# Performance work log

Hardware: AMD Instinct MI355X
Metric: run time of the kernel (lower is better)

The kernel has to match this reference:

```python
import jax, jax.numpy as jnp
import numpy as np

B, N, D, H, C = 8, 1024, 1024, 8, 1
S = 32            # sqrt(D // C): per-patch spatial map side
HD = D // H       # head dim = 128
SCALE = HD ** -0.5
BN_EPS = 1e-3     # Keras BatchNormalization default epsilon


def setup_inputs() -> dict:
    key = jax.random.key(0)
    ks = jax.random.split(key, 7)
    std = 0.02  # matches tf.random_normal_initializer(0.0, 0.02)
    return {
        "x": jax.random.normal(ks[0], (B, N, D), jnp.float32),
        "qw": jax.random.normal(ks[1], (3, 3, C, C), jnp.float32) * std,
        "kw": jax.random.normal(ks[2], (3, 3, C, C), jnp.float32) * std,
        "vw": jax.random.normal(ks[3], (3, 3, C, C), jnp.float32) * std,
        "reatten_w": jax.random.normal(ks[4], (N, N), jnp.float32) / np.float32(np.sqrt(N)),
        "reatten_b": jnp.zeros((N,), jnp.float32),
        "bn_gamma": jnp.ones((N,), jnp.float32),
        "bn_beta": jnp.zeros((N,), jnp.float32),
        "proj_w": jax.random.normal(ks[5], (D, D), jnp.float32) / np.float32(np.sqrt(D)),
        "proj_b": jnp.zeros((D,), jnp.float32),
    }


def _conv_qkv(x, w):
    # unflatten: [B, N, D] -> [B*N, S, S, C]; map_fn over batch with a shared
    # conv == one conv with B*N as batch dim. 3x3 SAME, no bias, exact GELU.
    xm = x.reshape(B * N, S, S, C)
    y = jax.lax.conv_general_dilated(
        xm, w, window_strides=(1, 1), padding='SAME',
        dimension_numbers=('NHWC', 'HWIO', 'NHWC'))
    y = jax.nn.gelu(y, approximate=False)
    # reshape to heads: [B, N, H, HD] -> [B, H, N, HD]
    return y.reshape(B, N, H, HD).transpose(0, 2, 1, 3)


def reference(x, qw, kw, vw, reatten_w, reatten_b, bn_gamma, bn_beta, proj_w, proj_b):
    q = _conv_qkv(x, qw)
    k = _conv_qkv(x, kw)
    v = _conv_qkv(x, vw)

    attn = jax.nn.softmax(jnp.einsum('bhid,bhjd->bhij', q, k) * SCALE, axis=-1)
    # re-attention: 1x1 conv over last (key) axis + BN (inference: mean=0, var=1)
    attn = jnp.einsum('bhic,cj->bhij', attn, reatten_w) + reatten_b
    attn = attn * (bn_gamma / jnp.sqrt(jnp.float32(1.0) + BN_EPS)) + bn_beta
    # reatten_scale = 1.0 (transform_scale=False)

    out = jnp.einsum('bhij,bhjd->bhid', attn, v)
    out = out.transpose(0, 2, 1, 3).reshape(B, N, D)
    out = out @ proj_w + proj_b
    return (out, attn)
```

## Files before the change

kernel.cpp:

```cpp
#include <hip/hip_runtime.h>
#include <hip/hip_bf16.h>

typedef __attribute__((ext_vector_type(8))) short short8;
typedef __attribute__((ext_vector_type(4))) float f32x4;

__device__ __forceinline__ void gload_lds16(const void* g, void* l) {
    __builtin_amdgcn_global_load_lds(
        (const __attribute__((address_space(1))) void*)g,
        (__attribute__((address_space(3))) void*)l, 16, 0, 0);
}

#define SBAR() do { __builtin_amdgcn_sched_barrier(0); __builtin_amdgcn_s_barrier(); __builtin_amdgcn_sched_barrier(0); } while (0)

__device__ __forceinline__ float gelu_exact(float x) {
    return 0.5f * x * (1.0f + erff(x * 0.70710678118654752f));
}
__device__ __forceinline__ float us2f(unsigned int u) {
    return __uint_as_float(u << 16);
}
__device__ __forceinline__ unsigned short f2b_raw(float f) {
    __hip_bfloat16 h = __float2bfloat16(f);
    return *reinterpret_cast<unsigned short*>(&h);
}
__device__ __forceinline__ float tofloat(float f) { return f; }
__device__ __forceinline__ float tofloat(__hip_bfloat16 h) { return __bfloat162float(h); }

__global__ __launch_bounds__(256) void conv_qkv(
    const float* __restrict__ x,
    const float* __restrict__ qw, const float* __restrict__ kw, const float* __restrict__ vw,
    __hip_bfloat16* __restrict__ qb, __hip_bfloat16* __restrict__ kb, __hip_bfloat16* __restrict__ vb)
{
    __shared__ float img[1024];
    const int bid = blockIdx.x;
    const int b = bid >> 10, n = bid & 1023;
    const float* xr = x + (long)bid * 1024;
    for (int i = threadIdx.x; i < 1024; i += 256) img[i] = xr[i];
    __syncthreads();

    float wq[9], wk[9], wv[9];
    #pragma unroll
    for (int i = 0; i < 9; ++i) { wq[i] = qw[i]; wk[i] = kw[i]; wv[i] = vw[i]; }

    for (int q = 0; q < 4; ++q) {
        const int p = q * 256 + threadIdx.x;
        const int r = p >> 5, c = p & 31;
        float sq = 0.f, sk = 0.f, sv = 0.f;
        #pragma unroll
        for (int dy = 0; dy < 3; ++dy) {
            const int rr = r + dy - 1;
            if (rr < 0 || rr > 31) continue;
            #pragma unroll
            for (int dx = 0; dx < 3; ++dx) {
                const int cc = c + dx - 1;
                if (cc < 0 || cc > 31) continue;
                const float px = img[rr * 32 + cc];
                sq += px * wq[dy * 3 + dx];
                sk += px * wk[dy * 3 + dx];
                sv += px * wv[dy * 3 + dx];
            }
        }
        sq = gelu_exact(sq); sk = gelu_exact(sk); sv = gelu_exact(sv);
        const int h = p >> 7, d = p & 127;
        const long off = ((long)(b * 8 + h) * 1024 + n) * 128 + d;
        qb[off] = __float2bfloat16(sq);
        kb[off] = __float2bfloat16(sk);
        vb[off] = __float2bfloat16(sv);
    }
}

template <typename Tin>
__global__ __launch_bounds__(256) void transpose_cast(
    const Tin* __restrict__ in, __hip_bfloat16* __restrict__ out,
    int R, int Cc, long inz, long outz)
{
    __shared__ float tile[32][33];
    const long z = blockIdx.z;
    const int c0 = blockIdx.x * 32, r0 = blockIdx.y * 32;
    const int tx = threadIdx.x & 31, ty = threadIdx.x >> 5;
    const Tin* ip = in + z * inz;
    #pragma unroll
    for (int i = 0; i < 32; i += 8)
        tile[ty + i][tx] = tofloat(ip[(long)(r0 + ty + i) * Cc + (c0 + tx)]);
    __syncthreads();
    __hip_bfloat16* op = out + z * outz;
    #pragma unroll
    for (int i = 0; i < 32; i += 8)
        op[(long)(c0 + ty + i) * R + (r0 + tx)] = __float2bfloat16(tile[tx][ty + i]);
}

__global__ __launch_bounds__(256) void softmax_inplace(__hip_bfloat16* __restrict__ S)
{
    __shared__ float red[8];
    const long row = blockIdx.x;
    uint2* p = reinterpret_cast<uint2*>(S + row * 1024);
    const int tid = threadIdx.x;
    uint2 u = p[tid];
    float v0 = us2f(u.x & 0xffffu), v1 = us2f(u.x >> 16);
    float v2 = us2f(u.y & 0xffffu), v3 = us2f(u.y >> 16);

    float m = fmaxf(fmaxf(v0, v1), fmaxf(v2, v3));
    for (int o = 32; o; o >>= 1) m = fmaxf(m, __shfl_xor(m, o));
    const int wave = tid >> 6, lane = tid & 63;
    if (lane == 0) red[wave] = m;
    __syncthreads();
    m = fmaxf(fmaxf(red[0], red[1]), fmaxf(red[2], red[3]));

    float e0 = expf(v0 - m), e1 = expf(v1 - m), e2 = expf(v2 - m), e3 = expf(v3 - m);
    float s = e0 + e1 + e2 + e3;
    for (int o = 32; o; o >>= 1) s += __shfl_xor(s, o);
    if (lane == 0) red[4 + wave] = s;
    __syncthreads();
    s = red[4] + red[5] + red[6] + red[7];
    const float inv = 1.0f / s;

    u.x = (unsigned int)f2b_raw(e0 * inv) | ((unsigned int)f2b_raw(e1 * inv) << 16);
    u.y = (unsigned int)f2b_raw(e2 * inv) | ((unsigned int)f2b_raw(e3 * inv) << 16);
    p[tid] = u;
}

__global__ __launch_bounds__(512, 2) void gemm_reatten_256(
    const __hip_bfloat16* __restrict__ Sall, const __hip_bfloat16* __restrict__ Wt,
    float* __restrict__ Cout,
    const float* __restrict__ bg, const float* __restrict__ rb, const float* __restrict__ bb)
{
    __shared__ __align__(16) char smem[131072];
    char* ldsA = smem;
    char* ldsB = smem + 65536;

    const int tid = threadIdx.x;
    const int z = blockIdx.z, tileM = blockIdx.x, tileN = blockIdx.y;
    const char* Ab = (const char*)(Sall + (long)z * 1048576 + (long)tileM * 256 * 1024);
    const char* Bb = (const char*)(Wt + (long)tileN * 256 * 1024);

    int grow[2], goff[2], pphys[2];
    #pragma unroll
    for (int i = 0; i < 2; ++i) {
        const int p = i * 8192 + tid * 16;
        const int l = p ^ (((p >> 7) & 3) << 4);
        pphys[i] = p; grow[i] = l >> 6; goff[i] = l & 63;
    }
    auto STAGE = [&](const char* gb, char* lb, int kt) {
        #pragma unroll
        for (int i = 0; i < 2; ++i)
            gload_lds16(gb + (long)grow[i] * 2048 + kt * 64 + goff[i], lb + pphys[i]);
    };

    const int lane = tid & 63, wid = tid >> 6;
    const int wrM = wid >> 2, wcn = wid & 3;
    const int fr = lane & 15, kl = lane >> 4;
    const int frbase = fr * 64 + kl * 16;

    auto LD8 = [&](const char* buf, int L) -> short8 {
        const int ph = L ^ (((L >> 7) & 3) << 4);
        return *(const short8*)(buf + ph);
    };

    f32x4 acc[8][4];
    #pragma unroll
    for (int m = 0; m < 8; ++m)
        #pragma unroll
        for (int n = 0; n < 4; ++n) acc[m][n] = (f32x4){0.f, 0.f, 0.f, 0.f};

    STAGE(Ab, ldsA, 0);          STAGE(Bb, ldsB, 0);
    STAGE(Ab, ldsA + 16384, 1);  STAGE(Bb, ldsB + 16384, 1);
    asm volatile("s_waitcnt vmcnt(4)" ::: "memory");
    SBAR();

    #pragma unroll 1
    for (int t = 0; t < 32; ++t) {
        char* bufA = ldsA + (t & 3) * 16384;
        char* bufB = ldsB + (t & 3) * 16384;
        const int t2 = t + 2;
        char* nA = ldsA + (t2 & 3) * 16384;
        char* nB = ldsB + (t2 & 3) * 16384;

        short8 bf[4], af[4];
        #pragma unroll
        for (int n = 0; n < 4; ++n) bf[n] = LD8(bufB, ((wcn * 64 + n * 16) * 64) + frbase);
        #pragma unroll
        for (int j = 0; j < 4; ++j) af[j] = LD8(bufA, ((wrM * 128 + j * 16) * 64) + frbase);
        if (t2 < 32) STAGE(Ab, nA, t2);
        SBAR();
        asm volatile("s_waitcnt lgkmcnt(0)" ::: "memory");
        __builtin_amdgcn_sched_barrier(0);
        __builtin_amdgcn_s_setprio(1);
        #pragma unroll
        for (int j = 0; j < 4; ++j)
            #pragma unroll
            for (int n = 0; n < 4; ++n)
                acc[j][n] = __builtin_amdgcn_mfma_f32_16x16x32_bf16(af[j], bf[n], acc[j][n], 0, 0, 0);
        __builtin_amdgcn_s_setprio(0);
        SBAR();

        #pragma unroll
        for (int j = 0; j < 4; ++j) af[j] = LD8(bufA, ((wrM * 128 + 64 + j * 16) * 64) + frbase);
        if (t2 < 32) STAGE(Bb, nB, t2);
        SBAR();
        asm volatile("s_waitcnt lgkmcnt(0)" ::: "memory");
        __builtin_amdgcn_sched_barrier(0);
        __builtin_amdgcn_s_setprio(1);
        #pragma unroll
        for (int j = 0; j < 4; ++j)
            #pragma unroll
            for (int n = 0; n < 4; ++n)
                acc[4 + j][n] = __builtin_amdgcn_mfma_f32_16x16x32_bf16(af[j], bf[n], acc[4 + j][n], 0, 0, 0);
        __builtin_amdgcn_s_setprio(0);
        if (t < 30)       asm volatile("s_waitcnt vmcnt(4)" ::: "memory");
        else if (t == 30) asm volatile("s_waitcnt vmcnt(0)" ::: "memory");
        SBAR();
    }

    __syncthreads();
    float* cbuf = (float*)smem;
    const float bninv = rsqrtf(1.0f + 1e-3f);
    float alpha[4], addv[4];
    #pragma unroll
    for (int n = 0; n < 4; ++n) {
        const int col = tileN * 256 + wcn * 64 + n * 16 + fr;
        const float g = bg[col];
        alpha[n] = g * bninv;
        addv[n] = rb[col] * alpha[n] + bb[col];
    }
    const int srow = tid >> 3, cseg = (tid & 7) * 4;
    #pragma unroll
    for (int c = 0; c < 4; ++c) {
        if (wrM == (c >> 1)) {
            #pragma unroll
            for (int j = 0; j < 4; ++j) {
                const int mf = (c & 1) * 4 + j;
                const int lrow0 = j * 16 + kl * 4;
                #pragma unroll
                for (int n = 0; n < 4; ++n)
                    #pragma unroll
                    for (int r = 0; r < 4; ++r)
                        cbuf[(lrow0 + r) * 260 + wcn * 64 + n * 16 + fr] =
                            acc[mf][n][r] * alpha[n] + addv[n];
            }
        }
        __syncthreads();
        float* gptr = Cout + (long)z * 1048576 +
                      (long)(tileM * 256 + c * 64 + srow) * 1024 + tileN * 256;
        #pragma unroll
        for (int i = 0; i < 8; ++i)
            *(f32x4*)(gptr + cseg + i * 32) = *(const f32x4*)&cbuf[srow * 260 + cseg + i * 32];
        __syncthreads();
    }
}

template <int MODE>
__global__ __launch_bounds__(256) void gemm_nt(
    const void* __restrict__ Aall, const __hip_bfloat16* __restrict__ Ball,
    void* __restrict__ Call, int K,
    long sAz, long sBz, long sCz,
    const float* __restrict__ e0)
{
    constexpr bool AF32 = (MODE == 2);
    constexpr bool OF32 = (MODE == 3);

    __shared__ __align__(16) char smem[32 * 132 * 4];
    short* As = (short*)smem;
    short* Bs = (short*)(smem + 8192);
    float* cbuf = (float*)smem;

    const int tid = threadIdx.x;
    const int z = blockIdx.z;
    const int tileM = blockIdx.x, tileN = blockIdx.y;

    const short* AwB = nullptr;
    const float* AwF = nullptr;
    if constexpr (AF32) AwF = (const float*)Aall + sAz * z + (long)tileM * 128 * K;
    else                AwB = (const short*)Aall + sAz * z + (long)tileM * 128 * K;
    const short* Bw = (const short*)Ball + sBz * z + (long)tileN * 128 * K;

    const int r0s = tid >> 2, k0s = (tid & 3) * 8;
    const int r1s = r0s + 64;

    f32x4 acc[4][4];
    #pragma unroll
    for (int m = 0; m < 4; ++m)
        #pragma unroll
        for (int n = 0; n < 4; ++n) acc[m][n] = (f32x4){0.f, 0.f, 0.f, 0.f};

    const int lane = tid & 63;
    const int wave = tid >> 6;
    const int wr = (wave >> 1) * 64, wc = (wave & 1) * 64;
    const int fr = lane & 15;
    const int kb = (lane >> 4) * 8;

    const int nk = K >> 5;
    for (int kt = 0; kt < nk; ++kt) {
        if constexpr (AF32) {
            const float* Ak0 = AwF + (long)r0s * K + kt * 32 + k0s;
            const float* Ak1 = AwF + (long)r1s * K + kt * 32 + k0s;
            f32x4 a00 = *(const f32x4*)Ak0;
            f32x4 a01 = *(const f32x4*)(Ak0 + 4);
            f32x4 a10 = *(const f32x4*)Ak1;
            f32x4 a11 = *(const f32x4*)(Ak1 + 4);
            __syncthreads();
            short8 s0, s1;
            #pragma unroll
            for (int i = 0; i < 4; ++i) {
                s0[i] = (short)f2b_raw(a00[i]); s0[i + 4] = (short)f2b_raw(a01[i]);
                s1[i] = (short)f2b_raw(a10[i]); s1[i + 4] = (short)f2b_raw(a11[i]);
            }
            *(short8*)&As[tid * 8] = s0;
            *(short8*)&As[(tid + 256) * 8] = s1;
            gload_lds16(Bw + (long)r0s * K + kt * 32 + k0s, &Bs[tid * 8]);
            gload_lds16(Bw + (long)r1s * K + kt * 32 + k0s, &Bs[(tid + 256) * 8]);
            __syncthreads();
        } else {
            __syncthreads();
            gload_lds16(AwB + (long)r0s * K + kt * 32 + k0s, &As[tid * 8]);
            gload_lds16(AwB + (long)r1s * K + kt * 32 + k0s, &As[(tid + 256) * 8]);
            gload_lds16(Bw + (long)r0s * K + kt * 32 + k0s, &Bs[tid * 8]);
            gload_lds16(Bw + (long)r1s * K + kt * 32 + k0s, &Bs[(tid + 256) * 8]);
            __syncthreads();
        }

        short8 af[4], bf[4];
        #pragma unroll
        for (int m = 0; m < 4; ++m) af[m] = *(const short8*)&As[(wr + m * 16 + fr) * 32 + kb];
        #pragma unroll
        for (int n = 0; n < 4; ++n) bf[n] = *(const short8*)&Bs[(wc + n * 16 + fr) * 32 + kb];
        #pragma unroll
        for (int m = 0; m < 4; ++m)
            #pragma unroll
            for (int n = 0; n < 4; ++n)
                acc[m][n] = __builtin_amdgcn_mfma_f32_16x16x32_bf16(af[m], bf[n], acc[m][n], 0, 0, 0);
    }

    long cbase;
    if (MODE == 2) cbase = (long)(z >> 3) * 1048576 + (long)(z & 7) * 128;
    else           cbase = sCz * z;

    float alpha[4], addv[4];
    #pragma unroll
    for (int n = 0; n < 4; ++n) {
        const int col = tileN * 128 + wc + n * 16 + fr;
        float a_ = 1.f, b_ = 0.f;
        if (MODE == 0) a_ = 0.08838834764831843f;
        if (MODE == 3) b_ = e0[col];
        alpha[n] = a_; addv[n] = b_;
    }

    __syncthreads();
    #pragma unroll
    for (int q = 0; q < 4; ++q) {
        if ((wave >> 1) == (q >> 1)) {
            #pragma unroll
            for (int mm = 0; mm < 2; ++mm) {
                const int m = (q & 1) * 2 + mm;
                const int lr0 = m * 16 + (lane >> 4) * 4 - (q & 1) * 32;
                #pragma unroll
                for (int n = 0; n < 4; ++n)
                    #pragma unroll
                    for (int r = 0; r < 4; ++r)
                        cbuf[(lr0 + r) * 132 + wc + n * 16 + fr] = acc[m][n][r] * alpha[n] + addv[n];
            }
        }
        __syncthreads();
        const long growbase = (long)tileM * 128 + q * 32;
        if constexpr (OF32) {
            float* Cg = (float*)Call + cbase;
            #pragma unroll
            for (int pass = 0; pass < 4; ++pass) {
                const int idx = (tid + pass * 256) * 4;
                const int row = idx >> 7, col = idx & 127;
                f32x4 v = *(const f32x4*)&cbuf[row * 132 + col];
                *(f32x4*)&Cg[(growbase + row) * 1024 + tileN * 128 + col] = v;
            }
        } else {
            __hip_bfloat16* Cg = (__hip_bfloat16*)Call + cbase;
            #pragma unroll
            for (int pass = 0; pass < 2; ++pass) {
                const int idx = (tid + pass * 256) * 8;
                const int row = idx >> 7, col = idx & 127;
                const float* src = &cbuf[row * 132 + col];
                f32x4 v0 = *(const f32x4*)src;
                f32x4 v1 = *(const f32x4*)(src + 4);
                short8 s;
                #pragma unroll
                for (int i = 0; i < 4; ++i) {
                    s[i] = (short)f2b_raw(v0[i]);
                    s[i + 4] = (short)f2b_raw(v1[i]);
                }
                *(short8*)&Cg[(growbase + row) * 1024 + tileN * 128 + col] = s;
            }
        }
        __syncthreads();
    }
}

extern "C" void kernel_launch(void* const* d_in, const int* in_sizes, int n_in,
                              void* d_out, int out_size, void* d_ws, size_t ws_size,
                              hipStream_t stream)
{
    const float* x  = (const float*)d_in[0];
    const float* qw = (const float*)d_in[1];
    const float* kw = (const float*)d_in[2];
    const float* vw = (const float*)d_in[3];
    const float* rw = (const float*)d_in[4];
    const float* rb = (const float*)d_in[5];
    const float* bg = (const float*)d_in[6];
    const float* bb = (const float*)d_in[7];
    const float* pw = (const float*)d_in[8];
    const float* pb = (const float*)d_in[9];

    float* outF  = (float*)d_out;
    float* attnF = outF + 8388608;

    char* w = (char*)d_ws;
    __hip_bfloat16* qb    = (__hip_bfloat16*)w; w += 16777216;
    __hip_bfloat16* kb    = (__hip_bfloat16*)w; w += 16777216;
    __hip_bfloat16* vb    = (__hip_bfloat16*)w; w += 16777216;
    __hip_bfloat16* vt    = (__hip_bfloat16*)w; w += 16777216;
    __hip_bfloat16* Wt    = (__hip_bfloat16*)w; w += 2097152;
    __hip_bfloat16* pWt   = (__hip_bfloat16*)w; w += 2097152;
    __hip_bfloat16* o2    = (__hip_bfloat16*)w; w += 16777216;
    __hip_bfloat16* S     = (__hip_bfloat16*)w; w += 134217728;

    conv_qkv<<<8192, 256, 0, stream>>>(x, qw, kw, vw, qb, kb, vb);
    transpose_cast<float><<<dim3(32, 32, 1), 256, 0, stream>>>(rw, Wt, 1024, 1024, 0, 0);
    transpose_cast<float><<<dim3(32, 32, 1), 256, 0, stream>>>(pw, pWt, 1024, 1024, 0, 0);
    transpose_cast<__hip_bfloat16><<<dim3(4, 32, 64), 256, 0, stream>>>(vb, vt, 1024, 128, 131072, 131072);

    gemm_nt<0><<<dim3(8, 8, 64), 256, 0, stream>>>(
        qb, kb, S, 128, 131072, 131072, 1048576, nullptr);
    softmax_inplace<<<65536, 256, 0, stream>>>(S);
    gemm_reatten_256<<<dim3(4, 4, 64), 512, 0, stream>>>(S, Wt, attnF, bg, rb, bb);
    gemm_nt<2><<<dim3(8, 1, 64), 256, 0, stream>>>(
        attnF, vt, o2, 1024, 1048576, 131072, 0, nullptr);
    gemm_nt<3><<<dim3(64, 8, 1), 256, 0, stream>>>(
        o2, pWt, outF, 1024, 0, 0, 0, pb);
}
```

Baseline: 423.8 us.

## Emit bf16 attention copy from re-attention GEMM and trim its barriers

The re-attention GEMM epilogue now also writes a bf16 copy of the attention matrix to a new 128 MB workspace buffer. The attn@V GEMM reads that copy with asynchronous global-to-LDS loads instead of loading fp32 attention and converting it in registers, so its fp32-path code is removed. The main loop of the re-attention GEMM also drops its intermediate barriers and explicit LDS waits, keeping one barrier per k-step and holding the second A-fragment half in separate registers. In exchange the epilogue stores an extra 128 MB of bf16 data and needs more workspace and registers, and correctness now depends on the four-deep LDS ring with a single barrier per step.

```diff
diff --git a/kernel.cpp b/kernel.cpp
--- a/kernel.cpp
+++ b/kernel.cpp
@@ -9,8 +9,6 @@
         (const __attribute__((address_space(1))) void*)g,
         (__attribute__((address_space(3))) void*)l, 16, 0, 0);
 }
-
-#define SBAR() do { __builtin_amdgcn_sched_barrier(0); __builtin_amdgcn_s_barrier(); __builtin_amdgcn_sched_barrier(0); } while (0)
 
 __device__ __forceinline__ float gelu_exact(float x) {
     return 0.5f * x * (1.0f + erff(x * 0.70710678118654752f));
@@ -120,7 +118,7 @@
 
 __global__ __launch_bounds__(512, 2) void gemm_reatten_256(
     const __hip_bfloat16* __restrict__ Sall, const __hip_bfloat16* __restrict__ Wt,
-    float* __restrict__ Cout,
+    float* __restrict__ Cout, __hip_bfloat16* __restrict__ C2out,
     const float* __restrict__ bg, const float* __restrict__ rb, const float* __restrict__ bb)
 {
     __shared__ __align__(16) char smem[131072];
@@ -164,7 +162,9 @@
     STAGE(Ab, ldsA, 0);          STAGE(Bb, ldsB, 0);
     STAGE(Ab, ldsA + 16384, 1);  STAGE(Bb, ldsB + 16384, 1);
     asm volatile("s_waitcnt vmcnt(4)" ::: "memory");
-    SBAR();
+    __builtin_amdgcn_sched_barrier(0);
+    __builtin_amdgcn_s_barrier();
+    __builtin_amdgcn_sched_barrier(0);
 
     #pragma unroll 1
     for (int t = 0; t < 32; ++t) {
@@ -174,15 +174,12 @@
         char* nA = ldsA + (t2 & 3) * 16384;
         char* nB = ldsB + (t2 & 3) * 16384;
 
-        short8 bf[4], af[4];
+        short8 bf[4], af[4], ag[4];
         #pragma unroll
         for (int n = 0; n < 4; ++n) bf[n] = LD8(bufB, ((wcn * 64 + n * 16) * 64) + frbase);
         #pragma unroll
         for (int j = 0; j < 4; ++j) af[j] = LD8(bufA, ((wrM * 128 + j * 16) * 64) + frbase);
         if (t2 < 32) STAGE(Ab, nA, t2);
-        SBAR();
-        asm volatile("s_waitcnt lgkmcnt(0)" ::: "memory");
-        __builtin_amdgcn_sched_barrier(0);
         __builtin_amdgcn_s_setprio(1);
         #pragma unroll
         for (int j = 0; j < 4; ++j)
@@ -190,24 +187,23 @@
             for (int n = 0; n < 4; ++n)
                 acc[j][n] = __builtin_amdgcn_mfma_f32_16x16x32_bf16(af[j], bf[n], acc[j][n], 0, 0, 0);
         __builtin_amdgcn_s_setprio(0);
-        SBAR();
-
-        #pragma unroll
-        for (int j = 0; j < 4; ++j) af[j] = LD8(bufA, ((wrM * 128 + 64 + j * 16) * 64) + frbase);
+
+        #pragma unroll
+        for (int j = 0; j < 4; ++j) ag[j] = LD8(bufA, ((wrM * 128 + 64 + j * 16) * 64) + frbase);
         if (t2 < 32) STAGE(Bb, nB, t2);
-        SBAR();
-        asm volatile("s_waitcnt lgkmcnt(0)" ::: "memory");
+        __builtin_amdgcn_s_setprio(1);
+        #pragma unroll
+        for (int j = 0; j < 4; ++j)
+            #pragma unroll
+            for (int n = 0; n < 4; ++n)
+                acc[4 + j][n] = __builtin_amdgcn_mfma_f32_16x16x32_bf16(ag[j], bf[n], acc[4 + j][n], 0, 0, 0);
+        __builtin_amdgcn_s_setprio(0);
+
+        if (t < 30)       { asm volatile("s_waitcnt vmcnt(4)" ::: "memory"); }
+        else if (t == 30) { asm volatile("s_waitcnt vmcnt(0)" ::: "memory"); }
         __builtin_amdgcn_sched_barrier(0);
-        __builtin_amdgcn_s_setprio(1);
-        #pragma unroll
-        for (int j = 0; j < 4; ++j)
-            #pragma unroll
-            for (int n = 0; n < 4; ++n)
-                acc[4 + j][n] = __builtin_amdgcn_mfma_f32_16x16x32_bf16(af[j], bf[n], acc[4 + j][n], 0, 0, 0);
-        __builtin_amdgcn_s_setprio(0);
-        if (t < 30)       asm volatile("s_waitcnt vmcnt(4)" ::: "memory");
-        else if (t == 30) asm volatile("s_waitcnt vmcnt(0)" ::: "memory");
-        SBAR();
+        __builtin_amdgcn_s_barrier();
+        __builtin_amdgcn_sched_barrier(0);
     }
 
     __syncthreads();
@@ -221,7 +217,7 @@
         alpha[n] = g * bninv;
         addv[n] = rb[col] * alpha[n] + bb[col];
     }
-    const int srow = tid >> 3, cseg = (tid & 7) * 4;
+    const int srow = tid >> 3, cseg = (tid & 7) * 4, c8 = (tid & 7) * 8;
     #pragma unroll
     for (int c = 0; c < 4; ++c) {
         if (wrM == (c >> 1)) {
@@ -238,23 +234,36 @@
             }
         }
         __syncthreads();
-        float* gptr = Cout + (long)z * 1048576 +
-                      (long)(tileM * 256 + c * 64 + srow) * 1024 + tileN * 256;
+        const long gro = (long)(tileM * 256 + c * 64 + srow);
+        float* gp = Cout + (long)z * 1048576 + gro * 1024 + tileN * 256;
         #pragma unroll
         for (int i = 0; i < 8; ++i)
-            *(f32x4*)(gptr + cseg + i * 32) = *(const f32x4*)&cbuf[srow * 260 + cseg + i * 32];
+            *(f32x4*)(gp + cseg + i * 32) = *(const f32x4*)&cbuf[srow * 260 + cseg + i * 32];
+        __hip_bfloat16* gp2 = C2out + (long)z * 1048576 + gro * 1024 + tileN * 256;
+        #pragma unroll
+        for (int i = 0; i < 4; ++i) {
+            const float* src = &cbuf[srow * 260 + c8 + i * 64];
+            f32x4 v0 = *(const f32x4*)src;
+            f32x4 v1 = *(const f32x4*)(src + 4);
+            short8 s;
+            #pragma unroll
+            for (int k = 0; k < 4; ++k) {
+                s[k] = (short)f2b_raw(v0[k]);
+                s[k + 4] = (short)f2b_raw(v1[k]);
+            }
+            *(short8*)(gp2 + c8 + i * 64) = s;
+        }
         __syncthreads();
     }
 }
 
 template <int MODE>
 __global__ __launch_bounds__(256) void gemm_nt(
-    const void* __restrict__ Aall, const __hip_bfloat16* __restrict__ Ball,
+    const __hip_bfloat16* __restrict__ Aall, const __hip_bfloat16* __restrict__ Ball,
     void* __restrict__ Call, int K,
     long sAz, long sBz, long sCz,
     const float* __restrict__ e0)
 {
-    constexpr bool AF32 = (MODE == 2);
     constexpr bool OF32 = (MODE == 3);
 
     __shared__ __align__(16) char smem[32 * 132 * 4];
@@ -266,10 +275,7 @@
     const int z = blockIdx.z;
     const int tileM = blockIdx.x, tileN = blockIdx.y;
 
-    const short* AwB = nullptr;
-    const float* AwF = nullptr;
-    if constexpr (AF32) AwF = (const float*)Aall + sAz * z + (long)tileM * 128 * K;
-    else                AwB = (const short*)Aall + sAz * z + (long)tileM * 128 * K;
+    const short* Aw = (const short*)Aall + sAz * z + (long)tileM * 128 * K;
     const short* Bw = (const short*)Ball + sBz * z + (long)tileN * 128 * K;
 
     const int r0s = tid >> 2, k0s = (tid & 3) * 8;
@@ -289,33 +295,12 @@
 
     const int nk = K >> 5;
     for (int kt = 0; kt < nk; ++kt) {
-        if constexpr (AF32) {
-            const float* Ak0 = AwF + (long)r0s * K + kt * 32 + k0s;
-            const float* Ak1 = AwF + (long)r1s * K + kt * 32 + k0s;
-            f32x4 a00 = *(const f32x4*)Ak0;
-            f32x4 a01 = *(const f32x4*)(Ak0 + 4);
-            f32x4 a10 = *(const f32x4*)Ak1;
-            f32x4 a11 = *(const f32x4*)(Ak1 + 4);
-            __syncthreads();
-            short8 s0, s1;
-            #pragma unroll
-            for (int i = 0; i < 4; ++i) {
-                s0[i] = (short)f2b_raw(a00[i]); s0[i + 4] = (short)f2b_raw(a01[i]);
-                s1[i] = (short)f2b_raw(a10[i]); s1[i + 4] = (short)f2b_raw(a11[i]);
-            }
-            *(short8*)&As[tid * 8] = s0;
-            *(short8*)&As[(tid + 256) * 8] = s1;
-            gload_lds16(Bw + (long)r0s * K + kt * 32 + k0s, &Bs[tid * 8]);
-            gload_lds16(Bw + (long)r1s * K + kt * 32 + k0s, &Bs[(tid + 256) * 8]);
-            __syncthreads();
-        } else {
-            __syncthreads();
-            gload_lds16(AwB + (long)r0s * K + kt * 32 + k0s, &As[tid * 8]);
-            gload_lds16(AwB + (long)r1s * K + kt * 32 + k0s, &As[(tid + 256) * 8]);
-            gload_lds16(Bw + (long)r0s * K + kt * 32 + k0s, &Bs[tid * 8]);
-            gload_lds16(Bw + (long)r1s * K + kt * 32 + k0s, &Bs[(tid + 256) * 8]);
-            __syncthreads();
-        }
+        __syncthreads();
+        gload_lds16(Aw + (long)r0s * K + kt * 32 + k0s, &As[tid * 8]);
+        gload_lds16(Aw + (long)r1s * K + kt * 32 + k0s, &As[(tid + 256) * 8]);
+        gload_lds16(Bw + (long)r0s * K + kt * 32 + k0s, &Bs[tid * 8]);
+        gload_lds16(Bw + (long)r1s * K + kt * 32 + k0s, &Bs[(tid + 256) * 8]);
+        __syncthreads();
 
         short8 af[4], bf[4];
         #pragma unroll
@@ -418,6 +403,7 @@
     __hip_bfloat16* pWt   = (__hip_bfloat16*)w; w += 2097152;
     __hip_bfloat16* o2    = (__hip_bfloat16*)w; w += 16777216;
     __hip_bfloat16* S     = (__hip_bfloat16*)w; w += 134217728;
+    __hip_bfloat16* attnb = (__hip_bfloat16*)w; w += 134217728;
 
     conv_qkv<<<8192, 256, 0, stream>>>(x, qw, kw, vw, qb, kb, vb);
     transpose_cast<float><<<dim3(32, 32, 1), 256, 0, stream>>>(rw, Wt, 1024, 1024, 0, 0);
@@ -427,9 +413,9 @@
     gemm_nt<0><<<dim3(8, 8, 64), 256, 0, stream>>>(
         qb, kb, S, 128, 131072, 131072, 1048576, nullptr);
     softmax_inplace<<<65536, 256, 0, stream>>>(S);
-    gemm_reatten_256<<<dim3(4, 4, 64), 512, 0, stream>>>(S, Wt, attnF, bg, rb, bb);
+    gemm_reatten_256<<<dim3(4, 4, 64), 512, 0, stream>>>(S, Wt, attnF, attnb, bg, rb, bb);
     gemm_nt<2><<<dim3(8, 1, 64), 256, 0, stream>>>(
-        attnF, vt, o2, 1024, 1048576, 131072, 0, nullptr);
+        attnb, vt, o2, 1024, 1048576, 131072, 0, nullptr);
     gemm_nt<3><<<dim3(64, 8, 1), 256, 0, stream>>>(
         o2, pWt, outF, 1024, 0, 0, 0, pb);
 }
```

Measured after the change: 405.9 us. -4.2%, faster.
